# Optimization experiments

Measured on AMD Instinct MI355X. Metric: run time of the kernel, lower is better.

Reference implementation:

```python
import jax, jax.numpy as jnp
import numpy as np

N_USER = 100000
N_ITEM = 50000
E = 1600000
D_USER = 128
D_ITEM = 64
H = 256


def setup_inputs() -> dict:
    key = jax.random.key(0)
    ks = jax.random.split(key, 20)
    w = lambda k, shape: (jax.random.normal(k, shape, jnp.float32) * 0.05)
    return {
        "x_user": jax.random.normal(ks[0], (N_USER, D_USER), jnp.float32),
        "x_item": jax.random.normal(ks[1], (N_ITEM, D_ITEM), jnp.float32),
        "edge_ui_src": jax.random.randint(ks[2], (E,), 0, N_USER, jnp.int32),
        "edge_ui_dst": jax.random.randint(ks[3], (E,), 0, N_ITEM, jnp.int32),
        "edge_iu_src": jax.random.randint(ks[4], (E,), 0, N_ITEM, jnp.int32),
        "edge_iu_dst": jax.random.randint(ks[5], (E,), 0, N_USER, jnp.int32),
        # layer 1 (per edge type): lin_l (src_dim->H, with bias), lin_r (dst_dim->H, no bias)
        "W1l_ui": w(ks[6], (H, D_USER)), "b1_ui": w(ks[7], (H,)), "W1r_ui": w(ks[8], (H, D_ITEM)),
        "W1l_iu": w(ks[9], (H, D_ITEM)), "b1_iu": w(ks[10], (H,)), "W1r_iu": w(ks[11], (H, D_USER)),
        # layer 2 (H -> H)
        "W2l_ui": w(ks[12], (H, H)), "b2_ui": w(ks[13], (H,)), "W2r_ui": w(ks[14], (H, H)),
        "W2l_iu": w(ks[15], (H, H)), "b2_iu": w(ks[16], (H,)), "W2r_iu": w(ks[17], (H, H)),
    }


def _sage_conv(x_src, x_dst, src, dst, Wl, b, Wr, n_dst):
    """PyG SAGEConv (aggr='mean', root_weight=True): lin_l(mean_j x_src[j]) + lin_r(x_dst)."""
    msg = x_src[src]                                                     # [E, Fs] gather
    s = jax.ops.segment_sum(msg, dst, num_segments=n_dst)                # [n_dst, Fs]
    cnt = jax.ops.segment_sum(jnp.ones((src.shape[0], 1), x_src.dtype), dst, num_segments=n_dst)
    mean = jnp.where(cnt > 0, s / jnp.maximum(cnt, 1.0), 0.0)            # isolated dst -> 0
    return mean @ Wl.T + b + x_dst @ Wr.T


def reference(x_user, x_item, edge_ui_src, edge_ui_dst, edge_iu_src, edge_iu_dst,
              W1l_ui, b1_ui, W1r_ui, W1l_iu, b1_iu, W1r_iu,
              W2l_ui, b2_ui, W2r_ui, W2l_iu, b2_iu, W2r_iu):
    # layer 1: one conv per edge type; to_hetero sums per dst type (single contributor here)
    h_item = _sage_conv(x_user, x_item, edge_ui_src, edge_ui_dst, W1l_ui, b1_ui, W1r_ui, N_ITEM)
    h_user = _sage_conv(x_item, x_user, edge_iu_src, edge_iu_dst, W1l_iu, b1_iu, W1r_iu, N_USER)
    h_item = jax.nn.relu(h_item)
    h_user = jax.nn.relu(h_user)
    # layer 2 (no activation after last layer in PyG BasicGNN)
    out_item = _sage_conv(h_user, h_item, edge_ui_src, edge_ui_dst, W2l_ui, b2_ui, W2r_ui, N_ITEM)
    out_user = _sage_conv(h_item, h_user, edge_iu_src, edge_iu_dst, W2l_iu, b2_iu, W2r_iu, N_USER)
    return out_user, out_item
```

## Files before the change

kernel.cpp:

```cpp
#include <hip/hip_runtime.h>


typedef unsigned short u16;
typedef unsigned int u32;
typedef short bf16x8 __attribute__((ext_vector_type(8)));
typedef float f32x4 __attribute__((ext_vector_type(4)));

constexpr int HDIM = 256;
constexpr int RB = 128;
constexpr int MAXB = 784;
constexpr int CHUNK = 4096;


__device__ __forceinline__ float lo2f(u32 v) { union { u32 i; float f; } x; x.i = v << 16; return x.f; }
__device__ __forceinline__ float hi2f(u32 v) { union { u32 i; float f; } x; x.i = v & 0xffff0000u; return x.f; }
__device__ __forceinline__ u16 f2bf(float f) {
    union { float f; u32 i; } x; x.f = f;
    return (u16)((x.i + 0x7fffu + ((x.i >> 16) & 1u)) >> 16);
}
__device__ __forceinline__ u32 pack2(float a, float b) {
    return (u32)f2bf(a) | ((u32)f2bf(b) << 16);
}

__device__ __forceinline__ void gload16(const void* g, void* l) {
    __builtin_amdgcn_global_load_lds(
        (const __attribute__((address_space(1))) unsigned int*)g,
        (__attribute__((address_space(3))) unsigned int*)l, 16, 0, 0);
}


__global__ __launch_bounds__(256) void bucket_count(const int* __restrict__ dst0, int nb0,
                                                    int* __restrict__ bc0,
                                                    const int* __restrict__ dst1, int nb1,
                                                    int* __restrict__ bc1,
                                                    int E, int sgrid) {
    __shared__ int lcnt[MAXB];
    int b = blockIdx.x;
    const int* dst; int nb; int* bc;
    if (b < sgrid) { dst = dst0; nb = nb0; bc = bc0; }
    else           { b -= sgrid; dst = dst1; nb = nb1; bc = bc1; }
    const int t = threadIdx.x;
    for (int i = t; i < nb; i += 256) lcnt[i] = 0;
    __syncthreads();
    const int base = b * CHUNK;
#pragma unroll
    for (int j = 0; j < CHUNK / 256; j++) {
        int i = base + j * 256 + t;
        if (i < E) atomicAdd(&lcnt[dst[i] >> 7], 1);
    }
    __syncthreads();
    for (int i = t; i < nb; i += 256) {
        int c = lcnt[i];
        if (c) atomicAdd(&bc[i], c);
    }
}

__global__ __launch_bounds__(1024) void bucket_scan(const int* __restrict__ bc0,
                                                    int* __restrict__ base0,
                                                    int* __restrict__ bcur0, int nb0,
                                                    const int* __restrict__ bc1,
                                                    int* __restrict__ base1,
                                                    int* __restrict__ bcur1, int nb1) {
    __shared__ int s[1024];
    const int t = threadIdx.x;
    int own = (t < nb0) ? bc0[t] : 0;
    s[t] = own;
    __syncthreads();
    for (int st = 1; st < 1024; st <<= 1) {
        int v = (t >= st) ? s[t - st] : 0;
        __syncthreads();
        s[t] += v;
        __syncthreads();
    }
    if (t < nb0) { int ex = s[t] - own; base0[t] = ex; bcur0[t] = ex; }
    if (t == 0) base0[nb0] = s[1023];
    __syncthreads();
    own = (t < nb1) ? bc1[t] : 0;
    s[t] = own;
    __syncthreads();
    for (int st = 1; st < 1024; st <<= 1) {
        int v = (t >= st) ? s[t - st] : 0;
        __syncthreads();
        s[t] += v;
        __syncthreads();
    }
    if (t < nb1) { int ex = s[t] - own; base1[t] = ex; bcur1[t] = ex; }
    if (t == 0) base1[nb1] = s[1023];
}

__global__ __launch_bounds__(256) void binned_scatter2(
    const int* __restrict__ src0, const int* __restrict__ dst0, int nb0,
    int* __restrict__ bcur0, uint2* __restrict__ pairs0,
    const int* __restrict__ src1, const int* __restrict__ dst1, int nb1,
    int* __restrict__ bcur1, uint2* __restrict__ pairs1,
    int E, int sgrid) {
    __shared__ int lcnt[MAXB];
    __shared__ int lbase[MAXB];
    int b = blockIdx.x;
    const int *src, *dst; int nb; int* bcur; uint2* pairs;
    if (b < sgrid) { src = src0; dst = dst0; nb = nb0; bcur = bcur0; pairs = pairs0; }
    else           { b -= sgrid; src = src1; dst = dst1; nb = nb1; bcur = bcur1; pairs = pairs1; }
    const int t = threadIdx.x;
    const int chunk = b * CHUNK;

    for (int i = t; i < nb; i += 256) lcnt[i] = 0;
    __syncthreads();

    u32 ss[CHUNK / 256], dd[CHUNK / 256];
#pragma unroll
    for (int j = 0; j < CHUNK / 256; j++) {
        int i = chunk + j * 256 + t;
        if (i < E) {
            ss[j] = (u32)src[i];
            dd[j] = (u32)dst[i];
            atomicAdd(&lcnt[dd[j] >> 7], 1);
        } else {
            ss[j] = 0; dd[j] = 0;
        }
    }
    __syncthreads();

    for (int i = t; i < nb; i += 256) {
        int c = lcnt[i];
        lbase[i] = (c > 0) ? atomicAdd(&bcur[i], c) : 0;
    }
    __syncthreads();
    for (int i = t; i < nb; i += 256) lcnt[i] = 0;
    __syncthreads();

#pragma unroll
    for (int j = 0; j < CHUNK / 256; j++) {
        int i = chunk + j * 256 + t;
        if (i < E) {
            int bb = (int)(dd[j] >> 7);
            int r = atomicAdd(&lcnt[bb], 1);
            pairs[(size_t)lbase[bb] + r] = make_uint2(ss[j], dd[j]);
        }
    }
}

__global__ __launch_bounds__(256) void bucket_fill2(
    const uint2* __restrict__ pairs0, const int* __restrict__ base0, int nb0, int n0,
    int* __restrict__ rp0, int* __restrict__ col0,
    const uint2* __restrict__ pairs1, const int* __restrict__ base1, int n1,
    int* __restrict__ rp1, int* __restrict__ col1) {
    __shared__ int rcnt[RB];
    __shared__ int excl[RB];
    __shared__ int lcur[RB];
    int b = blockIdx.x;
    const uint2* pairs; const int* bb; int n; int* rp; int* col;
    if (b < nb0) { pairs = pairs0; bb = base0; n = n0; rp = rp0; col = col0; }
    else         { b -= nb0; pairs = pairs1; bb = base1; n = n1; rp = rp1; col = col1; }
    const int t = threadIdx.x;
    const int r0 = b * RB;
    const int e0 = bb[b], e1 = bb[b + 1];

    if (t < RB) rcnt[t] = 0;
    __syncthreads();
    for (int j = e0 + t; j < e1; j += 256) atomicAdd(&rcnt[pairs[j].y & (RB - 1)], 1);
    __syncthreads();
    int own = (t < RB) ? rcnt[t] : 0;
    if (t < RB) excl[t] = own;
    __syncthreads();
    for (int st = 1; st < RB; st <<= 1) {
        int v = (t < RB && t >= st) ? excl[t - st] : 0;
        __syncthreads();
        if (t < RB) excl[t] += v;
        __syncthreads();
    }
    if (t < RB) {
        int ex = e0 + excl[t] - own;
        int row = r0 + t;
        if (row < n) rp[row] = ex;
        lcur[t] = ex;
    }
    if (t == 0 && r0 + RB >= n) rp[n] = e1;
    __syncthreads();
    for (int j = e0 + t; j < e1; j += 256) {
        uint2 e = pairs[j];
        int p = atomicAdd(&lcur[e.y & (RB - 1)], 1);
        col[p] = (int)e.x;
    }
}


struct ConvSeg { const float* in; u16* out; u32 n4; u32 pad; };
struct ConvArgs { ConvSeg s[10]; u32 tot; };

__global__ __launch_bounds__(256) void multi_convert(ConvArgs a) {
    for (u32 i = blockIdx.x * 256 + threadIdx.x; i < a.tot; i += gridDim.x * 256) {
        u32 r = i;
        int sg = 0;
        while (r >= a.s[sg].n4) { r -= a.s[sg].n4; sg++; }
        float4 v = ((const float4*)a.s[sg].in)[r];
        ((uint2*)a.s[sg].out)[r] = make_uint2(pack2(v.x, v.y), pack2(v.z, v.w));
    }
}


template <int F>
__device__ __forceinline__ void agg_row(const u16* __restrict__ src, const int* __restrict__ rp,
                                        const int* __restrict__ col, u16* __restrict__ out,
                                        int n_dst, int d) {
    constexpr int G = F / 8;
    constexpr int R = 64 / G;
    const int lane = threadIdx.x & 63;
    if (d >= n_dst) return;
    const int sub = lane / G;
    const int li = lane & (G - 1);
    const int e0 = rp[d], e1 = rp[d + 1];
    const size_t lo = (size_t)li * 8;

    float a[8] = {0.f, 0.f, 0.f, 0.f, 0.f, 0.f, 0.f, 0.f};
    auto add8 = [&](uint4 v) {
        a[0] += lo2f(v.x); a[1] += hi2f(v.x);
        a[2] += lo2f(v.y); a[3] += hi2f(v.y);
        a[4] += lo2f(v.z); a[5] += hi2f(v.z);
        a[6] += lo2f(v.w); a[7] += hi2f(v.w);
    };

    int ebase = e0;
    for (; ebase + 8 * R <= e1; ebase += 8 * R) {
        int c[8];
#pragma unroll
        for (int k = 0; k < 8; k++) c[k] = col[ebase + sub + k * R];
        uint4 v[8];
#pragma unroll
        for (int k = 0; k < 8; k++) v[k] = *(const uint4*)(src + (size_t)c[k] * F + lo);
#pragma unroll
        for (int k = 0; k < 8; k++) add8(v[k]);
    }
    for (; ebase + 4 * R <= e1; ebase += 4 * R) {
        int c[4];
#pragma unroll
        for (int k = 0; k < 4; k++) c[k] = col[ebase + sub + k * R];
        uint4 v[4];
#pragma unroll
        for (int k = 0; k < 4; k++) v[k] = *(const uint4*)(src + (size_t)c[k] * F + lo);
#pragma unroll
        for (int k = 0; k < 4; k++) add8(v[k]);
    }
    for (int e = ebase + sub; e < e1; e += R) {
        uint4 v = *(const uint4*)(src + (size_t)col[e] * F + lo);
        add8(v);
    }

#pragma unroll
    for (int m = G; m < 64; m <<= 1) {
#pragma unroll
        for (int j = 0; j < 8; j++) a[j] += __shfl_xor(a[j], m, 64);
    }

    const int deg = e1 - e0;
    const float inv = (deg > 0) ? 1.f / (float)deg : 0.f;
    if (lane < G) {
        uint4 w;
        w.x = pack2(a[0] * inv, a[1] * inv);
        w.y = pack2(a[2] * inv, a[3] * inv);
        w.z = pack2(a[4] * inv, a[5] * inv);
        w.w = pack2(a[6] * inv, a[7] * inv);
        *(uint4*)(out + (size_t)d * F + lo) = w;
    }
}

template <int F>
__global__ __launch_bounds__(256) void agg_mean(const u16* __restrict__ src,
                                                const int* __restrict__ rp,
                                                const int* __restrict__ col,
                                                u16* __restrict__ out, int n_dst) {
    agg_row<F>(src, rp, col, out, n_dst, blockIdx.x * 4 + (threadIdx.x >> 6));
}

__global__ __launch_bounds__(256) void agg_mean256_dual(
    const u16* __restrict__ src0, const int* __restrict__ rp0, const int* __restrict__ col0,
    u16* __restrict__ out0, int n0, int g0,
    const u16* __restrict__ src1, const int* __restrict__ rp1, const int* __restrict__ col1,
    u16* __restrict__ out1, int n1) {
    const int b = blockIdx.x;
    if (b < g0) agg_row<256>(src0, rp0, col0, out0, n0, b * 4 + (threadIdx.x >> 6));
    else        agg_row<256>(src1, rp1, col1, out1, n1, (b - g0) * 4 + (threadIdx.x >> 6));
}


template <int KA, int KB, bool RELU, bool OUT_BF16>
__global__ __launch_bounds__(256, 3) void gemm_tile(const u16* __restrict__ A,
                                                    const u16* __restrict__ X,
                                                    const u16* __restrict__ WA,
                                                    const u16* __restrict__ WB,
                                                    const float* __restrict__ bias,
                                                    float* __restrict__ outF,
                                                    u16* __restrict__ outB, int M) {
    constexpr int KT = KA + KB;
    constexpr int NKT = KT / 32;
    __shared__ __align__(16) u16 Al[128 * 32];
    __shared__ __align__(16) u16 Wl[128 * 32];

    const int nwg = gridDim.x;
    const int b = blockIdx.x;
    const int q = nwg >> 3, r = nwg & 7;
    const int xcd = b & 7, within = b >> 3;
    const int logical = (xcd < r ? xcd * (q + 1) : r * (q + 1) + (xcd - r) * q) + within;
    const int mb = logical >> 1;
    const int nb = logical & 1;
    const int row0 = mb * 128;
    const int ncol0 = nb * 128;

    const int tid = threadIdx.x;
    const int lane = tid & 63;
    const int wid = tid >> 6;
    const int wr = wid >> 1;
    const int wc = wid & 1;
    const int ml = lane & 15;
    const int ql = lane >> 4;
    const int lrow4 = lane >> 2;
    const int lcol8 = (lane & 3) * 8;

    f32x4 acc[4][4];
#pragma unroll
    for (int m = 0; m < 4; m++)
#pragma unroll
        for (int n = 0; n < 4; n++) acc[m][n] = {0.f, 0.f, 0.f, 0.f};

    const int s0 = wid * 2;

#pragma unroll
    for (int kt = 0; kt < NKT; ++kt) {
        const int kk = kt * 32;
#pragma unroll
        for (int j = 0; j < 2; ++j) {
            const int s = s0 + j;
            int gr = row0 + s * 16 + lrow4;
            gr = (gr < M) ? gr : (M - 1);
            const u16* gp = (kk < KA) ? (A + (size_t)gr * KA + (kk + lcol8))
                                      : (X + (size_t)gr * KB + (kk - KA + lcol8));
            gload16(gp, &Al[s * 512]);
        }
#pragma unroll
        for (int j = 0; j < 2; ++j) {
            const int s = s0 + j;
            const int gn = ncol0 + s * 16 + lrow4;
            const u16* gp = (kk < KA) ? (WA + (size_t)gn * KA + (kk + lcol8))
                                      : (WB + (size_t)gn * KB + (kk - KA + lcol8));
            gload16(gp, &Wl[s * 512]);
        }
        __syncthreads();

        bf16x8 af[4], wf[4];
#pragma unroll
        for (int m = 0; m < 4; m++)
            af[m] = *(const bf16x8*)&Al[(wr * 64 + m * 16 + ml) * 32 + ql * 8];
#pragma unroll
        for (int n = 0; n < 4; n++)
            wf[n] = *(const bf16x8*)&Wl[(wc * 64 + n * 16 + ml) * 32 + ql * 8];
#pragma unroll
        for (int m = 0; m < 4; m++)
#pragma unroll
            for (int n = 0; n < 4; n++)
                acc[m][n] = __builtin_amdgcn_mfma_f32_16x16x32_bf16(af[m], wf[n], acc[m][n], 0, 0, 0);
        __syncthreads();
    }

#pragma unroll
    for (int n = 0; n < 4; n++) {
        const int gcol = ncol0 + wc * 64 + n * 16 + ml;
        const float bv = bias[gcol];
#pragma unroll
        for (int m = 0; m < 4; m++) {
            const int gr0 = row0 + wr * 64 + m * 16 + ql * 4;
#pragma unroll
            for (int rr = 0; rr < 4; rr++) {
                const int grow = gr0 + rr;
                if (grow >= M) continue;
                float v = acc[m][n][rr] + bv;
                if (RELU) v = fmaxf(v, 0.f);
                if (OUT_BF16) outB[(size_t)grow * HDIM + gcol] = f2bf(v);
                else          outF[(size_t)grow * HDIM + gcol] = v;
            }
        }
    }
}


extern "C" void kernel_launch(void* const* d_in, const int* in_sizes, int n_in,
                              void* d_out, int out_size, void* d_ws, size_t ws_size,
                              hipStream_t stream) {
    const float* x_user = (const float*)d_in[0];
    const float* x_item = (const float*)d_in[1];
    const int* eui_src = (const int*)d_in[2];
    const int* eui_dst = (const int*)d_in[3];
    const int* eiu_src = (const int*)d_in[4];
    const int* eiu_dst = (const int*)d_in[5];
    const float* W1l_ui = (const float*)d_in[6];
    const float* b1_ui  = (const float*)d_in[7];
    const float* W1r_ui = (const float*)d_in[8];
    const float* W1l_iu = (const float*)d_in[9];
    const float* b1_iu  = (const float*)d_in[10];
    const float* W1r_iu = (const float*)d_in[11];
    const float* W2l_ui = (const float*)d_in[12];
    const float* b2_ui  = (const float*)d_in[13];
    const float* W2r_ui = (const float*)d_in[14];
    const float* W2l_iu = (const float*)d_in[15];
    const float* b2_iu  = (const float*)d_in[16];
    const float* W2r_iu = (const float*)d_in[17];

    const int DU = 128, DI = 64;
    const int NU = in_sizes[0] / DU;
    const int NI = in_sizes[1] / DI;
    const int E  = in_sizes[2];

    char* base = (char*)d_ws;
    size_t off = 0;
    auto carve = [&](size_t bytes) -> char* {
        char* p = base + off;
        off += (bytes + 255) & ~(size_t)255;
        return p;
    };
    int* rp_i   = (int*)carve((size_t)(NI + 1) * 4);
    int* rp_u   = (int*)carve((size_t)(NU + 1) * 4);
    int* col_ui = (int*)carve((size_t)E * 4);
    int* col_iu = (int*)carve((size_t)E * 4);
    int* bc     = (int*)carve((size_t)2 * MAXB * 4);
    int* bc_i   = bc;
    int* bc_u   = bc + MAXB;
    int* base_i = (int*)carve((size_t)(MAXB + 1) * 4);
    int* base_u = (int*)carve((size_t)(MAXB + 1) * 4);
    int* bcur_i = (int*)carve(MAXB * 4);
    int* bcur_u = (int*)carve(MAXB * 4);
    u16* W1l_ui_b = (u16*)carve((size_t)HDIM * DU * 2);
    u16* W1r_ui_b = (u16*)carve((size_t)HDIM * DI * 2);
    u16* W1l_iu_b = (u16*)carve((size_t)HDIM * DI * 2);
    u16* W1r_iu_b = (u16*)carve((size_t)HDIM * DU * 2);
    u16* W2l_ui_b = (u16*)carve((size_t)HDIM * HDIM * 2);
    u16* W2r_ui_b = (u16*)carve((size_t)HDIM * HDIM * 2);
    u16* W2l_iu_b = (u16*)carve((size_t)HDIM * HDIM * 2);
    u16* W2r_iu_b = (u16*)carve((size_t)HDIM * HDIM * 2);
    char* slot1 = carve((size_t)NU * DU * 2);
    u16* x_user_b = (u16*)slot1;
    u16* B_i      = (u16*)slot1;
    char* slotB = carve((size_t)NU * HDIM * 2);
    u16* x_item_b = (u16*)slotB;
    u16* A_i      = (u16*)(slotB + (size_t)NI * DI * 2);
    u16* A_u      = (u16*)(slotB + (size_t)NI * DI * 2 + (size_t)NI * DU * 2);
    u16* B_u      = (u16*)slotB;
    u16* h_item_b = (u16*)carve((size_t)NI * HDIM * 2);
    u16* h_user_b = (u16*)carve((size_t)NU * HDIM * 2);

    uint2* pairs_i = (uint2*)h_user_b;
    uint2* pairs_u = (uint2*)(h_user_b + (size_t)E * 4);

    float* out_user = (float*)d_out;
    float* out_item = (float*)d_out + (size_t)NU * HDIM;

    const int nb_i = (NI + RB - 1) / RB;
    const int nb_u = (NU + RB - 1) / RB;
    const int sgrid = (E + CHUNK - 1) / CHUNK;

    hipMemsetAsync(bc, 0, (size_t)2 * MAXB * 4, stream);
    bucket_count<<<2 * sgrid, 256, 0, stream>>>(eui_dst, nb_i, bc_i, eiu_dst, nb_u, bc_u, E, sgrid);
    bucket_scan<<<1, 1024, 0, stream>>>(bc_i, base_i, bcur_i, nb_i, bc_u, base_u, bcur_u, nb_u);
    binned_scatter2<<<2 * sgrid, 256, 0, stream>>>(
        eui_src, eui_dst, nb_i, bcur_i, pairs_i,
        eiu_src, eiu_dst, nb_u, bcur_u, pairs_u, E, sgrid);
    bucket_fill2<<<nb_i + nb_u, 256, 0, stream>>>(
        pairs_i, base_i, nb_i, NI, rp_i, col_ui,
        pairs_u, base_u, NU, rp_u, col_iu);

    {
        ConvArgs ca;
        auto seg = [&](int i, const float* in, u16* outp, size_t n) {
            ca.s[i].in = in; ca.s[i].out = outp; ca.s[i].n4 = (u32)(n / 4); ca.s[i].pad = 0;
        };
        seg(0, x_user, x_user_b, (size_t)NU * DU);
        seg(1, x_item, x_item_b, (size_t)NI * DI);
        seg(2, W2l_ui, W2l_ui_b, (size_t)HDIM * HDIM);
        seg(3, W2r_ui, W2r_ui_b, (size_t)HDIM * HDIM);
        seg(4, W2l_iu, W2l_iu_b, (size_t)HDIM * HDIM);
        seg(5, W2r_iu, W2r_iu_b, (size_t)HDIM * HDIM);
        seg(6, W1l_ui, W1l_ui_b, (size_t)HDIM * DU);
        seg(7, W1r_ui, W1r_ui_b, (size_t)HDIM * DI);
        seg(8, W1l_iu, W1l_iu_b, (size_t)HDIM * DI);
        seg(9, W1r_iu, W1r_iu_b, (size_t)HDIM * DU);
        u32 tot = 0;
        for (int i = 0; i < 10; i++) tot += ca.s[i].n4;
        ca.tot = tot;
        multi_convert<<<2048, 256, 0, stream>>>(ca);
    }

    agg_mean<128><<<(NI + 3) / 4, 256, 0, stream>>>(x_user_b, rp_i, col_ui, A_i, NI);
    agg_mean<64> <<<(NU + 3) / 4, 256, 0, stream>>>(x_item_b, rp_u, col_iu, A_u, NU);
    {
        int gi = ((NI + 127) / 128) * 2;
        int gu = ((NU + 127) / 128) * 2;
        gemm_tile<128, 64, true, true><<<gi, 256, 0, stream>>>(
            A_i, x_item_b, W1l_ui_b, W1r_ui_b, b1_ui, nullptr, h_item_b, NI);
        gemm_tile<64, 128, true, true><<<gu, 256, 0, stream>>>(
            A_u, x_user_b, W1l_iu_b, W1r_iu_b, b1_iu, nullptr, h_user_b, NU);
    }

    {
        int gi = (NI + 3) / 4;
        int gu = (NU + 3) / 4;
        agg_mean256_dual<<<gi + gu, 256, 0, stream>>>(
            h_user_b, rp_i, col_ui, B_i, NI, gi,
            h_item_b, rp_u, col_iu, B_u, NU);
    }
    {
        int gi = ((NI + 127) / 128) * 2;
        int gu = ((NU + 127) / 128) * 2;
        gemm_tile<256, 256, false, false><<<gi, 256, 0, stream>>>(
            B_i, h_item_b, W2l_ui_b, W2r_ui_b, b2_ui, out_item, nullptr, NI);
        gemm_tile<256, 256, false, false><<<gu, 256, 0, stream>>>(
            B_u, h_user_b, W2l_iu_b, W2r_iu_b, b2_iu, out_user, nullptr, NU);
    }
}
```

Baseline: 824.8 us.

## Split hidden features into column halves, pack edge pairs, fuse layer-2 GEMMs

Layer-1 outputs are stored as two 128-column halves so the layer-2 aggregation runs as two 128-wide gather passes with smaller per-pass working sets, aiming for better cache hit rates on random gathers. Edge pairs are packed into one 32-bit word (src<<7 | row-in-bucket) to halve scatter/fill traffic. The layer-1 aggregations become one dual launch. The two layer-2 GEMMs are merged into a single launch with XCD-aware block remapping. The cost is an extra pass over the CSR indices, and the packed word limits src ids to 25 bits.

Result: slower. 862.0 us (+4.5%).

```diff
diff --git a/kernel.cpp b/kernel.cpp
--- a/kernel.cpp
+++ b/kernel.cpp
@@ -90,14 +90,14 @@
 
 __global__ __launch_bounds__(256) void binned_scatter2(
     const int* __restrict__ src0, const int* __restrict__ dst0, int nb0,
-    int* __restrict__ bcur0, uint2* __restrict__ pairs0,
+    int* __restrict__ bcur0, u32* __restrict__ pairs0,
     const int* __restrict__ src1, const int* __restrict__ dst1, int nb1,
-    int* __restrict__ bcur1, uint2* __restrict__ pairs1,
+    int* __restrict__ bcur1, u32* __restrict__ pairs1,
     int E, int sgrid) {
     __shared__ int lcnt[MAXB];
     __shared__ int lbase[MAXB];
     int b = blockIdx.x;
-    const int *src, *dst; int nb; int* bcur; uint2* pairs;
+    const int *src, *dst; int nb; int* bcur; u32* pairs;
     if (b < sgrid) { src = src0; dst = dst0; nb = nb0; bcur = bcur0; pairs = pairs0; }
     else           { b -= sgrid; src = src1; dst = dst1; nb = nb1; bcur = bcur1; pairs = pairs1; }
     const int t = threadIdx.x;
@@ -134,21 +134,21 @@
         if (i < E) {
             int bb = (int)(dd[j] >> 7);
             int r = atomicAdd(&lcnt[bb], 1);
-            pairs[(size_t)lbase[bb] + r] = make_uint2(ss[j], dd[j]);
+            pairs[(size_t)lbase[bb] + r] = (ss[j] << 7) | (dd[j] & 127u);
         }
     }
 }
 
 __global__ __launch_bounds__(256) void bucket_fill2(
-    const uint2* __restrict__ pairs0, const int* __restrict__ base0, int nb0, int n0,
+    const u32* __restrict__ pairs0, const int* __restrict__ base0, int nb0, int n0,
     int* __restrict__ rp0, int* __restrict__ col0,
-    const uint2* __restrict__ pairs1, const int* __restrict__ base1, int n1,
+    const u32* __restrict__ pairs1, const int* __restrict__ base1, int n1,
     int* __restrict__ rp1, int* __restrict__ col1) {
     __shared__ int rcnt[RB];
     __shared__ int excl[RB];
     __shared__ int lcur[RB];
     int b = blockIdx.x;
-    const uint2* pairs; const int* bb; int n; int* rp; int* col;
+    const u32* pairs; const int* bb; int n; int* rp; int* col;
     if (b < nb0) { pairs = pairs0; bb = base0; n = n0; rp = rp0; col = col0; }
     else         { b -= nb0; pairs = pairs1; bb = base1; n = n1; rp = rp1; col = col1; }
     const int t = threadIdx.x;
@@ -157,7 +157,7 @@
 
     if (t < RB) rcnt[t] = 0;
     __syncthreads();
-    for (int j = e0 + t; j < e1; j += 256) atomicAdd(&rcnt[pairs[j].y & (RB - 1)], 1);
+    for (int j = e0 + t; j < e1; j += 256) atomicAdd(&rcnt[pairs[j] & (RB - 1)], 1);
     __syncthreads();
     int own = (t < RB) ? rcnt[t] : 0;
     if (t < RB) excl[t] = own;
@@ -177,9 +177,9 @@
     if (t == 0 && r0 + RB >= n) rp[n] = e1;
     __syncthreads();
     for (int j = e0 + t; j < e1; j += 256) {
-        uint2 e = pairs[j];
-        int p = atomicAdd(&lcur[e.y & (RB - 1)], 1);
-        col[p] = (int)e.x;
+        u32 e = pairs[j];
+        int p = atomicAdd(&lcur[e & (RB - 1)], 1);
+        col[p] = (int)(e >> 7);
     }
 }
 
@@ -263,33 +263,26 @@
     }
 }
 
-template <int F>
-__global__ __launch_bounds__(256) void agg_mean(const u16* __restrict__ src,
-                                                const int* __restrict__ rp,
-                                                const int* __restrict__ col,
-                                                u16* __restrict__ out, int n_dst) {
-    agg_row<F>(src, rp, col, out, n_dst, blockIdx.x * 4 + (threadIdx.x >> 6));
-}
-
-__global__ __launch_bounds__(256) void agg_mean256_dual(
+template <int F0, int F1>
+__global__ __launch_bounds__(256) void agg_dual(
     const u16* __restrict__ src0, const int* __restrict__ rp0, const int* __restrict__ col0,
     u16* __restrict__ out0, int n0, int g0,
     const u16* __restrict__ src1, const int* __restrict__ rp1, const int* __restrict__ col1,
     u16* __restrict__ out1, int n1) {
     const int b = blockIdx.x;
-    if (b < g0) agg_row<256>(src0, rp0, col0, out0, n0, b * 4 + (threadIdx.x >> 6));
-    else        agg_row<256>(src1, rp1, col1, out1, n1, (b - g0) * 4 + (threadIdx.x >> 6));
-}
-
-
-template <int KA, int KB, bool RELU, bool OUT_BF16>
-__global__ __launch_bounds__(256, 3) void gemm_tile(const u16* __restrict__ A,
-                                                    const u16* __restrict__ X,
-                                                    const u16* __restrict__ WA,
-                                                    const u16* __restrict__ WB,
-                                                    const float* __restrict__ bias,
-                                                    float* __restrict__ outF,
-                                                    u16* __restrict__ outB, int M) {
+    if (b < g0) agg_row<F0>(src0, rp0, col0, out0, n0, b * 4 + (threadIdx.x >> 6));
+    else        agg_row<F1>(src1, rp1, col1, out1, n1, (b - g0) * 4 + (threadIdx.x >> 6));
+}
+
+
+template <int KA, int KB>
+__global__ __launch_bounds__(256, 3) void gemm_l1(const u16* __restrict__ A,
+                                                  const u16* __restrict__ X,
+                                                  const u16* __restrict__ WA,
+                                                  const u16* __restrict__ WB,
+                                                  const float* __restrict__ bias,
+                                                  u16* __restrict__ outLo,
+                                                  u16* __restrict__ outHi, int M) {
     constexpr int KT = KA + KB;
     constexpr int NKT = KT / 32;
     __shared__ __align__(16) u16 Al[128 * 32];
@@ -364,6 +357,9 @@
     for (int n = 0; n < 4; n++) {
         const int gcol = ncol0 + wc * 64 + n * 16 + ml;
         const float bv = bias[gcol];
+        u16* ob; int cw;
+        if (gcol < 128) { ob = outLo; cw = gcol; }
+        else            { ob = outHi; cw = gcol - 128; }
 #pragma unroll
         for (int m = 0; m < 4; m++) {
             const int gr0 = row0 + wr * 64 + m * 16 + ql * 4;
@@ -371,10 +367,105 @@
             for (int rr = 0; rr < 4; rr++) {
                 const int grow = gr0 + rr;
                 if (grow >= M) continue;
-                float v = acc[m][n][rr] + bv;
-                if (RELU) v = fmaxf(v, 0.f);
-                if (OUT_BF16) outB[(size_t)grow * HDIM + gcol] = f2bf(v);
-                else          outF[(size_t)grow * HDIM + gcol] = v;
+                float v = fmaxf(acc[m][n][rr] + bv, 0.f);
+                ob[(size_t)grow * 128 + cw] = f2bf(v);
+            }
+        }
+    }
+}
+
+struct GemmSet {
+    const u16* p0; const u16* p1; const u16* p2; const u16* p3;
+    const u16* WA; const u16* WB;
+    const float* bias; float* out; int M; int pad;
+};
+struct GemmL2Args { GemmSet s[2]; int g0; };
+
+__global__ __launch_bounds__(256, 3) void gemm_l2(GemmL2Args a) {
+    __shared__ __align__(16) u16 Al[128 * 32];
+    __shared__ __align__(16) u16 Wl[128 * 32];
+
+    const int nwg = gridDim.x;
+    const int b = blockIdx.x;
+    const int q = nwg >> 3, r = nwg & 7;
+    const int xcd = b & 7, within = b >> 3;
+    int logical = (xcd < r ? xcd * (q + 1) : r * (q + 1) + (xcd - r) * q) + within;
+    const GemmSet& S = (logical < a.g0) ? a.s[0] : a.s[1];
+    if (logical >= a.g0) logical -= a.g0;
+    const int mb = logical >> 1;
+    const int nb = logical & 1;
+    const int row0 = mb * 128;
+    const int ncol0 = nb * 128;
+    const int M = S.M;
+    const u16* srcs[4] = {S.p0, S.p1, S.p2, S.p3};
+
+    const int tid = threadIdx.x;
+    const int lane = tid & 63;
+    const int wid = tid >> 6;
+    const int wr = wid >> 1;
+    const int wc = wid & 1;
+    const int ml = lane & 15;
+    const int ql = lane >> 4;
+    const int lrow4 = lane >> 2;
+    const int lcol8 = (lane & 3) * 8;
+
+    f32x4 acc[4][4];
+#pragma unroll
+    for (int m = 0; m < 4; m++)
+#pragma unroll
+        for (int n = 0; n < 4; n++) acc[m][n] = {0.f, 0.f, 0.f, 0.f};
+
+    const int s0 = wid * 2;
+
+#pragma unroll
+    for (int kt = 0; kt < 16; ++kt) {
+        const int kk = kt * 32;
+        const int sel = kt >> 2;
+        const int off = kk & 127;
+#pragma unroll
+        for (int j = 0; j < 2; ++j) {
+            const int s = s0 + j;
+            int gr = row0 + s * 16 + lrow4;
+            gr = (gr < M) ? gr : (M - 1);
+            gload16(srcs[sel] + (size_t)gr * 128 + off + lcol8, &Al[s * 512]);
+        }
+#pragma unroll
+        for (int j = 0; j < 2; ++j) {
+            const int s = s0 + j;
+            const int gn = ncol0 + s * 16 + lrow4;
+            const u16* wp = (kt < 8) ? (S.WA + (size_t)gn * 256 + kk + lcol8)
+                                     : (S.WB + (size_t)gn * 256 + (kk - 256 + lcol8));
+            gload16(wp, &Wl[s * 512]);
+        }
+        __syncthreads();
+
+        bf16x8 af[4], wf[4];
+#pragma unroll
+        for (int m = 0; m < 4; m++)
+            af[m] = *(const bf16x8*)&Al[(wr * 64 + m * 16 + ml) * 32 + ql * 8];
+#pragma unroll
+        for (int n = 0; n < 4; n++)
+            wf[n] = *(const bf16x8*)&Wl[(wc * 64 + n * 16 + ml) * 32 + ql * 8];
+#pragma unroll
+        for (int m = 0; m < 4; m++)
+#pragma unroll
+            for (int n = 0; n < 4; n++)
+                acc[m][n] = __builtin_amdgcn_mfma_f32_16x16x32_bf16(af[m], wf[n], acc[m][n], 0, 0, 0);
+        __syncthreads();
+    }
+
+#pragma unroll
+    for (int n = 0; n < 4; n++) {
+        const int gcol = ncol0 + wc * 64 + n * 16 + ml;
+        const float bv = S.bias[gcol];
+#pragma unroll
+        for (int m = 0; m < 4; m++) {
+            const int gr0 = row0 + wr * 64 + m * 16 + ql * 4;
+#pragma unroll
+            for (int rr = 0; rr < 4; rr++) {
+                const int grow = gr0 + rr;
+                if (grow >= M) continue;
+                S.out[(size_t)grow * HDIM + gcol] = acc[m][n][rr] + bv;
             }
         }
     }
@@ -436,17 +527,21 @@
     u16* W2r_iu_b = (u16*)carve((size_t)HDIM * HDIM * 2);
     char* slot1 = carve((size_t)NU * DU * 2);
     u16* x_user_b = (u16*)slot1;
-    u16* B_i      = (u16*)slot1;
+    u16* B_i_lo   = (u16*)slot1;
+    u16* B_i_hi   = (u16*)(slot1 + (size_t)NI * 128 * 2);
     char* slotB = carve((size_t)NU * HDIM * 2);
     u16* x_item_b = (u16*)slotB;
     u16* A_i      = (u16*)(slotB + (size_t)NI * DI * 2);
     u16* A_u      = (u16*)(slotB + (size_t)NI * DI * 2 + (size_t)NI * DU * 2);
-    u16* B_u      = (u16*)slotB;
-    u16* h_item_b = (u16*)carve((size_t)NI * HDIM * 2);
-    u16* h_user_b = (u16*)carve((size_t)NU * HDIM * 2);
-
-    uint2* pairs_i = (uint2*)h_user_b;
-    uint2* pairs_u = (uint2*)(h_user_b + (size_t)E * 4);
+    u16* B_u_lo   = (u16*)slotB;
+    u16* B_u_hi   = (u16*)(slotB + (size_t)NU * 128 * 2);
+    u16* h_item_lo = (u16*)carve((size_t)NI * 128 * 2);
+    u16* h_item_hi = (u16*)carve((size_t)NI * 128 * 2);
+    u16* h_user_lo = (u16*)carve((size_t)NU * 128 * 2);
+    u16* h_user_hi = (u16*)carve((size_t)NU * 128 * 2);
+
+    u32* pairs_i = (u32*)h_user_lo;
+    u32* pairs_u = pairs_i + E;
 
     float* out_user = (float*)d_out;
     float* out_item = (float*)d_out + (size_t)NU * HDIM;
@@ -486,30 +581,34 @@
         multi_convert<<<2048, 256, 0, stream>>>(ca);
     }
 
-    agg_mean<128><<<(NI + 3) / 4, 256, 0, stream>>>(x_user_b, rp_i, col_ui, A_i, NI);
-    agg_mean<64> <<<(NU + 3) / 4, 256, 0, stream>>>(x_item_b, rp_u, col_iu, A_u, NU);
+    const int gi = (NI + 3) / 4;
+    const int gu = (NU + 3) / 4;
+
+    agg_dual<128, 64><<<gi + gu, 256, 0, stream>>>(
+        x_user_b, rp_i, col_ui, A_i, NI, gi,
+        x_item_b, rp_u, col_iu, A_u, NU);
+    gemm_l1<128, 64><<<((NI + 127) / 128) * 2, 256, 0, stream>>>(
+        A_i, x_item_b, W1l_ui_b, W1r_ui_b, b1_ui, h_item_lo, h_item_hi, NI);
+    gemm_l1<64, 128><<<((NU + 127) / 128) * 2, 256, 0, stream>>>(
+        A_u, x_user_b, W1l_iu_b, W1r_iu_b, b1_iu, h_user_lo, h_user_hi, NU);
+
+    agg_dual<128, 128><<<gi + gu, 256, 0, stream>>>(
+        h_user_lo, rp_i, col_ui, B_i_lo, NI, gi,
+        h_item_lo, rp_u, col_iu, B_u_lo, NU);
+    agg_dual<128, 128><<<gi + gu, 256, 0, stream>>>(
+        h_user_hi, rp_i, col_ui, B_i_hi, NI, gi,
+        h_item_hi, rp_u, col_iu, B_u_hi, NU);
     {
-        int gi = ((NI + 127) / 128) * 2;
-        int gu = ((NU + 127) / 128) * 2;
-        gemm_tile<128, 64, true, true><<<gi, 256, 0, stream>>>(
-            A_i, x_item_b, W1l_ui_b, W1r_ui_b, b1_ui, nullptr, h_item_b, NI);
-        gemm_tile<64, 128, true, true><<<gu, 256, 0, stream>>>(
-            A_u, x_user_b, W1l_iu_b, W1r_iu_b, b1_iu, nullptr, h_user_b, NU);
-    }
-
-    {
-        int gi = (NI + 3) / 4;
-        int gu = (NU + 3) / 4;
-        agg_mean256_dual<<<gi + gu, 256, 0, stream>>>(
-            h_user_b, rp_i, col_ui, B_i, NI, gi,
-            h_item_b, rp_u, col_iu, B_u, NU);
-    }
-    {
-        int gi = ((NI + 127) / 128) * 2;
-        int gu = ((NU + 127) / 128) * 2;
-        gemm_tile<256, 256, false, false><<<gi, 256, 0, stream>>>(
-            B_i, h_item_b, W2l_ui_b, W2r_ui_b, b2_ui, out_item, nullptr, NI);
-        gemm_tile<256, 256, false, false><<<gu, 256, 0, stream>>>(
-            B_u, h_user_b, W2l_iu_b, W2r_iu_b, b2_iu, out_user, nullptr, NU);
-    }
-}
+        GemmL2Args ga;
+        ga.s[0].p0 = B_i_lo; ga.s[0].p1 = B_i_hi; ga.s[0].p2 = h_item_lo; ga.s[0].p3 = h_item_hi;
+        ga.s[0].WA = W2l_ui_b; ga.s[0].WB = W2r_ui_b; ga.s[0].bias = b2_ui;
+        ga.s[0].out = out_item; ga.s[0].M = NI; ga.s[0].pad = 0;
+        ga.s[1].p0 = B_u_lo; ga.s[1].p1 = B_u_hi; ga.s[1].p2 = h_user_lo; ga.s[1].p3 = h_user_hi;
+        ga.s[1].WA = W2l_iu_b; ga.s[1].WB = W2r_iu_b; ga.s[1].bias = b2_iu;
+        ga.s[1].out = out_user; ga.s[1].M = NU; ga.s[1].pad = 0;
+        int g0 = ((NI + 127) / 128) * 2;
+        int g1 = ((NU + 127) / 128) * 2;
+        ga.g0 = g0;
+        gemm_l2<<<g0 + g1, 256, 0, stream>>>(ga);
+    }
+}
```

## Co-schedule GEMM tiles with independent aggregations in fused kernels and compact edge pairs

Applied to the files above, without the earlier changes.

Introduces a fused kernel that interleaves GEMM tile blocks with mean-aggregation blocks that do not depend on each other, so the bandwidth-bound gathers and the compute-bound matmuls share the GPU at the same time. The stages are re-chained so each aggregation runs alongside the previous GEMM, which lets the total kernel count fall. It also packs the src index and the low 7 bits of dst into one u32 for the binning pairs, halving that scratch traffic. It drops the XCD-aware block remapping from the GEMM, changes the launch bounds (no minimum of 3 blocks), and adds a separate B_u buffer, which could affect occupancy and cache locality.

Result: slower. 1.031 ms (+25.0%).

```diff
diff --git a/kernel.cpp b/kernel.cpp
--- a/kernel.cpp
+++ b/kernel.cpp
@@ -90,14 +90,14 @@
 
 __global__ __launch_bounds__(256) void binned_scatter2(
     const int* __restrict__ src0, const int* __restrict__ dst0, int nb0,
-    int* __restrict__ bcur0, uint2* __restrict__ pairs0,
+    int* __restrict__ bcur0, u32* __restrict__ pairs0,
     const int* __restrict__ src1, const int* __restrict__ dst1, int nb1,
-    int* __restrict__ bcur1, uint2* __restrict__ pairs1,
+    int* __restrict__ bcur1, u32* __restrict__ pairs1,
     int E, int sgrid) {
     __shared__ int lcnt[MAXB];
     __shared__ int lbase[MAXB];
     int b = blockIdx.x;
-    const int *src, *dst; int nb; int* bcur; uint2* pairs;
+    const int *src, *dst; int nb; int* bcur; u32* pairs;
     if (b < sgrid) { src = src0; dst = dst0; nb = nb0; bcur = bcur0; pairs = pairs0; }
     else           { b -= sgrid; src = src1; dst = dst1; nb = nb1; bcur = bcur1; pairs = pairs1; }
     const int t = threadIdx.x;
@@ -134,21 +134,21 @@
         if (i < E) {
             int bb = (int)(dd[j] >> 7);
             int r = atomicAdd(&lcnt[bb], 1);
-            pairs[(size_t)lbase[bb] + r] = make_uint2(ss[j], dd[j]);
+            pairs[(size_t)lbase[bb] + r] = (ss[j] << 7) | (dd[j] & 127u);
         }
     }
 }
 
 __global__ __launch_bounds__(256) void bucket_fill2(
-    const uint2* __restrict__ pairs0, const int* __restrict__ base0, int nb0, int n0,
+    const u32* __restrict__ pairs0, const int* __restrict__ base0, int nb0, int n0,
     int* __restrict__ rp0, int* __restrict__ col0,
-    const uint2* __restrict__ pairs1, const int* __restrict__ base1, int n1,
+    const u32* __restrict__ pairs1, const int* __restrict__ base1, int n1,
     int* __restrict__ rp1, int* __restrict__ col1) {
     __shared__ int rcnt[RB];
     __shared__ int excl[RB];
     __shared__ int lcur[RB];
     int b = blockIdx.x;
-    const uint2* pairs; const int* bb; int n; int* rp; int* col;
+    const u32* pairs; const int* bb; int n; int* rp; int* col;
     if (b < nb0) { pairs = pairs0; bb = base0; n = n0; rp = rp0; col = col0; }
     else         { b -= nb0; pairs = pairs1; bb = base1; n = n1; rp = rp1; col = col1; }
     const int t = threadIdx.x;
@@ -157,7 +157,7 @@
 
     if (t < RB) rcnt[t] = 0;
     __syncthreads();
-    for (int j = e0 + t; j < e1; j += 256) atomicAdd(&rcnt[pairs[j].y & (RB - 1)], 1);
+    for (int j = e0 + t; j < e1; j += 256) atomicAdd(&rcnt[pairs[j] & (RB - 1)], 1);
     __syncthreads();
     int own = (t < RB) ? rcnt[t] : 0;
     if (t < RB) excl[t] = own;
@@ -177,9 +177,9 @@
     if (t == 0 && r0 + RB >= n) rp[n] = e1;
     __syncthreads();
     for (int j = e0 + t; j < e1; j += 256) {
-        uint2 e = pairs[j];
-        int p = atomicAdd(&lcur[e.y & (RB - 1)], 1);
-        col[p] = (int)e.x;
+        u32 e = pairs[j];
+        int p = atomicAdd(&lcur[e & (RB - 1)], 1);
+        col[p] = (int)(e >> 7);
     }
 }
 
@@ -263,45 +263,20 @@
     }
 }
 
-template <int F>
-__global__ __launch_bounds__(256) void agg_mean(const u16* __restrict__ src,
-                                                const int* __restrict__ rp,
-                                                const int* __restrict__ col,
-                                                u16* __restrict__ out, int n_dst) {
-    agg_row<F>(src, rp, col, out, n_dst, blockIdx.x * 4 + (threadIdx.x >> 6));
-}
-
-__global__ __launch_bounds__(256) void agg_mean256_dual(
-    const u16* __restrict__ src0, const int* __restrict__ rp0, const int* __restrict__ col0,
-    u16* __restrict__ out0, int n0, int g0,
-    const u16* __restrict__ src1, const int* __restrict__ rp1, const int* __restrict__ col1,
-    u16* __restrict__ out1, int n1) {
-    const int b = blockIdx.x;
-    if (b < g0) agg_row<256>(src0, rp0, col0, out0, n0, b * 4 + (threadIdx.x >> 6));
-    else        agg_row<256>(src1, rp1, col1, out1, n1, (b - g0) * 4 + (threadIdx.x >> 6));
-}
-
 
 template <int KA, int KB, bool RELU, bool OUT_BF16>
-__global__ __launch_bounds__(256, 3) void gemm_tile(const u16* __restrict__ A,
-                                                    const u16* __restrict__ X,
-                                                    const u16* __restrict__ WA,
-                                                    const u16* __restrict__ WB,
-                                                    const float* __restrict__ bias,
-                                                    float* __restrict__ outF,
-                                                    u16* __restrict__ outB, int M) {
+__device__ __forceinline__ void gemm_body(int vb, u16* Al, u16* Wl,
+                                          const u16* __restrict__ A,
+                                          const u16* __restrict__ X,
+                                          const u16* __restrict__ WA,
+                                          const u16* __restrict__ WB,
+                                          const float* __restrict__ bias,
+                                          float* __restrict__ outF,
+                                          u16* __restrict__ outB, int M) {
     constexpr int KT = KA + KB;
     constexpr int NKT = KT / 32;
-    __shared__ __align__(16) u16 Al[128 * 32];
-    __shared__ __align__(16) u16 Wl[128 * 32];
-
-    const int nwg = gridDim.x;
-    const int b = blockIdx.x;
-    const int q = nwg >> 3, r = nwg & 7;
-    const int xcd = b & 7, within = b >> 3;
-    const int logical = (xcd < r ? xcd * (q + 1) : r * (q + 1) + (xcd - r) * q) + within;
-    const int mb = logical >> 1;
-    const int nb = logical & 1;
+    const int mb = vb >> 1;
+    const int nb = vb & 1;
     const int row0 = mb * 128;
     const int ncol0 = nb * 128;
 
@@ -377,6 +352,40 @@
                 else          outF[(size_t)grow * HDIM + gcol] = v;
             }
         }
+    }
+}
+
+
+struct FusedArgs {
+    const u16* A; const u16* X; const u16* WA; const u16* WB;
+    const float* gbias; float* outF; u16* outB; int M; int n_g;
+    const u16* asrc; const int* arp; const int* acol; u16* aout; int a_n; int n_a;
+    int S; int pad;
+};
+
+template <int KA, int KB, bool RELU, bool OUT_BF16, int F>
+__global__ __launch_bounds__(256) void fused_ga(FusedArgs a) {
+    __shared__ __align__(16) u16 Al[128 * 32];
+    __shared__ __align__(16) u16 Wl[128 * 32];
+    const int b = blockIdx.x;
+    bool isg; int id;
+    if (a.n_a == 0)      { isg = true;  id = b; }
+    else if (a.n_g == 0) { isg = false; id = b; }
+    else {
+        const int qq = b / a.S;
+        if (b % a.S == 0 && qq < a.n_g) { isg = true; id = qq; }
+        else {
+            int before = qq + 1;
+            if (before > a.n_g) before = a.n_g;
+            isg = false; id = b - before;
+        }
+    }
+    if (isg) {
+        gemm_body<KA, KB, RELU, OUT_BF16>(id, Al, Wl, a.A, a.X, a.WA, a.WB,
+                                          a.gbias, a.outF, a.outB, a.M);
+    } else {
+        agg_row<F>(a.asrc, a.arp, a.acol, a.aout, a.a_n,
+                   id * 4 + ((int)threadIdx.x >> 6));
     }
 }
 
@@ -434,19 +443,19 @@
     u16* W2r_ui_b = (u16*)carve((size_t)HDIM * HDIM * 2);
     u16* W2l_iu_b = (u16*)carve((size_t)HDIM * HDIM * 2);
     u16* W2r_iu_b = (u16*)carve((size_t)HDIM * HDIM * 2);
-    char* slot1 = carve((size_t)NU * DU * 2);
-    u16* x_user_b = (u16*)slot1;
-    u16* B_i      = (u16*)slot1;
-    char* slotB = carve((size_t)NU * HDIM * 2);
-    u16* x_item_b = (u16*)slotB;
-    u16* A_i      = (u16*)(slotB + (size_t)NI * DI * 2);
-    u16* A_u      = (u16*)(slotB + (size_t)NI * DI * 2 + (size_t)NI * DU * 2);
-    u16* B_u      = (u16*)slotB;
-    u16* h_item_b = (u16*)carve((size_t)NI * HDIM * 2);
-    u16* h_user_b = (u16*)carve((size_t)NU * HDIM * 2);
-
-    uint2* pairs_i = (uint2*)h_user_b;
-    uint2* pairs_u = (uint2*)(h_user_b + (size_t)E * 4);
+    char* reg1 = carve((size_t)NU * DU * 2);
+    u16* x_user_b = (u16*)reg1;
+    u16* B_i      = (u16*)reg1;
+    char* reg2 = carve((size_t)NI * DI * 2 + (size_t)NI * DU * 2 + (size_t)NU * DI * 2);
+    u16* x_item_b = (u16*)reg2;
+    u16* A_i      = (u16*)(reg2 + (size_t)NI * DI * 2);
+    u16* A_u      = (u16*)(reg2 + (size_t)NI * DI * 2 + (size_t)NI * DU * 2);
+    u16* B_u    = (u16*)carve((size_t)NU * HDIM * 2);
+    u16* h_item = (u16*)carve((size_t)NI * HDIM * 2);
+    u16* h_user = (u16*)carve((size_t)NU * HDIM * 2);
+
+    u32* pairs_i = (u32*)h_user;
+    u32* pairs_u = pairs_i + E;
 
     float* out_user = (float*)d_out;
     float* out_item = (float*)d_out + (size_t)NU * HDIM;
@@ -486,30 +495,50 @@
         multi_convert<<<2048, 256, 0, stream>>>(ca);
     }
 
-    agg_mean<128><<<(NI + 3) / 4, 256, 0, stream>>>(x_user_b, rp_i, col_ui, A_i, NI);
-    agg_mean<64> <<<(NU + 3) / 4, 256, 0, stream>>>(x_item_b, rp_u, col_iu, A_u, NU);
-    {
-        int gi = ((NI + 127) / 128) * 2;
-        int gu = ((NU + 127) / 128) * 2;
-        gemm_tile<128, 64, true, true><<<gi, 256, 0, stream>>>(
-            A_i, x_item_b, W1l_ui_b, W1r_ui_b, b1_ui, nullptr, h_item_b, NI);
-        gemm_tile<64, 128, true, true><<<gu, 256, 0, stream>>>(
-            A_u, x_user_b, W1l_iu_b, W1r_iu_b, b1_iu, nullptr, h_user_b, NU);
-    }
-
-    {
-        int gi = (NI + 3) / 4;
-        int gu = (NU + 3) / 4;
-        agg_mean256_dual<<<gi + gu, 256, 0, stream>>>(
-            h_user_b, rp_i, col_ui, B_i, NI, gi,
-            h_item_b, rp_u, col_iu, B_u, NU);
-    }
-    {
-        int gi = ((NI + 127) / 128) * 2;
-        int gu = ((NU + 127) / 128) * 2;
-        gemm_tile<256, 256, false, false><<<gi, 256, 0, stream>>>(
-            B_i, h_item_b, W2l_ui_b, W2r_ui_b, b2_ui, out_item, nullptr, NI);
-        gemm_tile<256, 256, false, false><<<gu, 256, 0, stream>>>(
-            B_u, h_user_b, W2l_iu_b, W2r_iu_b, b2_iu, out_user, nullptr, NU);
-    }
-}
+    const int gi = (NI + 3) / 4;
+    const int gu = (NU + 3) / 4;
+    const int ng_i = ((NI + 127) / 128) * 2;
+    const int ng_u = ((NU + 127) / 128) * 2;
+
+    auto mkS = [](int n_g, int n_a) -> int {
+        if (n_g == 0 || n_a == 0) return 1;
+        int S = (n_g + n_a) / n_g;
+        if (S < 1) S = 1;
+        if (S > 1 && (S & 1) == 0) S -= 1;
+        return S;
+    };
+    FusedArgs fa;
+
+    fa = {};
+    fa.n_g = 0;
+    fa.asrc = x_user_b; fa.arp = rp_i; fa.acol = col_ui; fa.aout = A_i; fa.a_n = NI; fa.n_a = gi;
+    fa.S = 1;
+    fused_ga<128, 64, true, true, 128><<<gi, 256, 0, stream>>>(fa);
+
+    fa = {};
+    fa.A = A_i; fa.X = x_item_b; fa.WA = W1l_ui_b; fa.WB = W1r_ui_b; fa.gbias = b1_ui;
+    fa.outF = nullptr; fa.outB = h_item; fa.M = NI; fa.n_g = ng_i;
+    fa.asrc = x_item_b; fa.arp = rp_u; fa.acol = col_iu; fa.aout = A_u; fa.a_n = NU; fa.n_a = gu;
+    fa.S = mkS(ng_i, gu);
+    fused_ga<128, 64, true, true, 64><<<ng_i + gu, 256, 0, stream>>>(fa);
+
+    fa = {};
+    fa.A = A_u; fa.X = x_user_b; fa.WA = W1l_iu_b; fa.WB = W1r_iu_b; fa.gbias = b1_iu;
+    fa.outF = nullptr; fa.outB = h_user; fa.M = NU; fa.n_g = ng_u;
+    fa.asrc = h_item; fa.arp = rp_u; fa.acol = col_iu; fa.aout = B_u; fa.a_n = NU; fa.n_a = gu;
+    fa.S = mkS(ng_u, gu);
+    fused_ga<64, 128, true, true, 256><<<ng_u + gu, 256, 0, stream>>>(fa);
+
+    fa = {};
+    fa.A = B_u; fa.X = h_user; fa.WA = W2l_iu_b; fa.WB = W2r_iu_b; fa.gbias = b2_iu;
+    fa.outF = out_user; fa.outB = nullptr; fa.M = NU; fa.n_g = ng_u;
+    fa.asrc = h_user; fa.arp = rp_i; fa.acol = col_ui; fa.aout = B_i; fa.a_n = NI; fa.n_a = gi;
+    fa.S = mkS(ng_u, gi);
+    fused_ga<256, 256, false, false, 256><<<ng_u + gi, 256, 0, stream>>>(fa);
+
+    fa = {};
+    fa.A = B_i; fa.X = h_item; fa.WA = W2l_ui_b; fa.WB = W2r_ui_b; fa.gbias = b2_ui;
+    fa.outF = out_item; fa.outB = nullptr; fa.M = NI; fa.n_g = ng_i;
+    fa.n_a = 0; fa.S = 1;
+    fused_ga<256, 256, false, false, 256><<<ng_i, 256, 0, stream>>>(fa);
+}
```
